# Kernel optimization log

Measured on AMD Instinct MI355X. Metric: run time of the kernel, lower is better.

## Reference

```python
import jax, jax.numpy as jnp
import numpy as np

N = 100000      # nodes
E = 1600000     # edges (unique, no self-loops)
DIN = 128
DOUT = 128


def _make_edges():
    """Unique undirected edges, no self-loops, ring guarantees min degree 2.
    Ensures dense-adjacency semantics == edge-list segment-sum semantics."""
    rng = np.random.default_rng(0)
    ring = np.stack([np.arange(N, dtype=np.int64), (np.arange(N, dtype=np.int64) + 1) % N], axis=1)
    ring = np.sort(ring, axis=1)  # canonical (min,max)
    ring_keys = ring[:, 0] * N + ring[:, 1]
    cand = rng.integers(0, N, size=(3 * E, 2), dtype=np.int64)
    cand = cand[cand[:, 0] != cand[:, 1]]
    cand = np.sort(cand, axis=1)
    keys = cand[:, 0] * N + cand[:, 1]
    _, idx = np.unique(keys, return_index=True)
    cand = cand[np.sort(idx)]
    cand = cand[~np.isin(cand[:, 0] * N + cand[:, 1], ring_keys)][: E - N]
    edges = np.concatenate([ring, cand], axis=0)  # [E, 2]
    return edges.T  # [2, E]


def setup_inputs() -> dict:
    key = jax.random.key(0)
    kx, kw = jax.random.split(key)
    X = jax.random.normal(kx, (N, DIN), dtype=jnp.float32)
    # kaiming_normal_ default (fan_in mode): std = sqrt(2 / fan_in)
    W = jax.random.normal(kw, (DIN, DOUT), dtype=jnp.float32) * np.float32(np.sqrt(2.0 / DIN))
    edge_list = jnp.asarray(_make_edges(), dtype=jnp.int64)
    return {"X": X, "W": W, "edge_list": edge_list}


def reference(X, W, edge_list):
    src, dst = edge_list[0], edge_list[1]
    n = X.shape[0]
    ones = jnp.ones(src.shape[0], dtype=X.dtype)
    # D: each edge increments both endpoint degrees (matches the torch loop)
    deg = jnp.zeros((n,), X.dtype).at[src].add(ones).at[dst].add(ones)
    # A_hat @ X = symmetric neighbor aggregation + self (identity)
    agg = jnp.zeros_like(X).at[dst].add(X[src]).at[src].add(X[dst]) + X
    # D^-1 is inverse of diagonal -> elementwise reciprocal
    z = (agg / deg[:, None]) @ W
    return jax.nn.relu(z)
```

## Files before the change

kernel.cpp:

```cpp
#include <hip/hip_runtime.h>
#include <hip/hip_fp16.h>


#define DFEAT 128
#define BSH 7
#define BNODES (1 << BSH)
#define NBMAX 800
#define EPT_SC 4
#define EPB (1024 * EPT_SC)
#define SORT_CAP 6144

typedef __attribute__((ext_vector_type(8))) short short8;
typedef __attribute__((ext_vector_type(4))) float f32x4;

__device__ __forceinline__ unsigned short f2bf(float x) {
  unsigned u = __float_as_uint(x);
  return (unsigned short)((u + 0x7FFFu + ((u >> 16) & 1u)) >> 16);
}
__device__ __forceinline__ __half2 u2h(unsigned x) {
  union { unsigned u; __half2 h; } c; c.u = x; return c.h;
}
__device__ __forceinline__ unsigned h2u(__half2 x) {
  union { __half2 h; unsigned u; } c; c.h = x; return c.u;
}

__global__ void init_kernel(const int* el32, int* gcur, int* flag, int NB) {
  int i = blockIdx.x * blockDim.x + threadIdx.x;
  if (i < NB) gcur[i] = 0;
  if (i == 0) flag[0] = (el32[1] == 0 && el32[3] == 0) ? 1 : 0;
}

__device__ __forceinline__ int edge_at(const void* el, long long i, int mode64) {
  if (mode64) return (int)((const long long*)el)[i];
  return ((const int*)el)[i];
}

__global__ __launch_bounds__(1024) void scatter_kernel(const void* el,
                                                       const int* __restrict__ flag,
                                                       int* __restrict__ gcur,
                                                       unsigned int* __restrict__ bucket,
                                                       int E, int NB) {
  __shared__ int lh[NBMAX];
  __shared__ int lb[NBMAX];
  int t = threadIdx.x;
  for (int i = t; i < NB; i += 1024) lh[i] = 0;
  __syncthreads();
  int m = flag[0];
  long long e0 = (long long)blockIdx.x * EPB + t;
  int s[EPT_SC], d[EPT_SC];
#pragma unroll
  for (int r = 0; r < EPT_SC; r++) {
    long long e = e0 + r * 1024;
    if (e < E) {
      s[r] = edge_at(el, e, m);
      d[r] = edge_at(el, (long long)E + e, m);
    } else {
      s[r] = -1;
    }
  }
#pragma unroll
  for (int r = 0; r < EPT_SC; r++) {
    if (s[r] >= 0) {
      atomicAdd(&lh[s[r] >> BSH], 1);
      atomicAdd(&lh[d[r] >> BSH], 1);
    }
  }
  __syncthreads();
  for (int i = t; i < NB; i += 1024) {
    int c = lh[i];
    lb[i] = c ? atomicAdd(&gcur[i], c) : 0;
  }
  __syncthreads();
  for (int i = t; i < NB; i += 1024) lh[i] = 0;
  __syncthreads();
#pragma unroll
  for (int r = 0; r < EPT_SC; r++) {
    if (s[r] >= 0) {
      int bs = s[r] >> BSH, bd = d[r] >> BSH;
      int ps = lb[bs] + atomicAdd(&lh[bs], 1);
      if (ps < SORT_CAP)
        bucket[(long long)bs * SORT_CAP + ps] =
            ((unsigned)(s[r] & (BNODES - 1)) << 20) | (unsigned)d[r];
      int pd = lb[bd] + atomicAdd(&lh[bd], 1);
      if (pd < SORT_CAP)
        bucket[(long long)bd * SORT_CAP + pd] =
            ((unsigned)(d[r] & (BNODES - 1)) << 20) | (unsigned)s[r];
    }
  }
}

__global__ __launch_bounds__(1024) void sort_kernel(const unsigned int* __restrict__ bucket,
                                                    const int* __restrict__ gcur,
                                                    int* __restrict__ adj,
                                                    int* __restrict__ start,
                                                    int* __restrict__ degg,
                                                    int n) {
  __shared__ int srt[SORT_CAP];
  __shared__ int h[BNODES], pref[BNODES], cur[BNODES], scn[BNODES];
  int b = blockIdx.x, t = threadIdx.x;
  int cnt = gcur[b]; if (cnt > SORT_CAP) cnt = SORT_CAP;
  long long base = (long long)b * SORT_CAP;

  if (t < BNODES) h[t] = 0;
  __syncthreads();
  for (int i = t; i < cnt; i += 1024)
    atomicAdd(&h[bucket[base + i] >> 20], 1);
  __syncthreads();
  int v = (t < BNODES) ? h[t] : 0;
  if (t < BNODES) scn[t] = v;
  __syncthreads();
  for (int dd = 1; dd < BNODES; dd <<= 1) {
    int a = (t < BNODES && t >= dd) ? scn[t - dd] : 0;
    __syncthreads();
    if (t < BNODES) scn[t] += a;
    __syncthreads();
  }
  if (t < BNODES) { pref[t] = scn[t] - v; cur[t] = scn[t] - v; }
  __syncthreads();
  for (int i = t; i < cnt; i += 1024) {
    unsigned e = bucket[base + i];
    int p = atomicAdd(&cur[e >> 20], 1);
    srt[p] = (int)(e & 0xFFFFFu);
  }
  __syncthreads();
  for (int i = t; i < cnt; i += 1024) adj[base + i] = srt[i];
  int node = (b << BSH) + t;
  if (t < BNODES && node < n) {
    start[node] = (int)(base + pref[t]);
    degg[node] = h[t];
  }
}

__global__ __launch_bounds__(256) void wfrag_kernel(const float* __restrict__ W,
                                                    unsigned int* __restrict__ Wfrag) {
  int e = blockIdx.x * 256 + threadIdx.x;
  if (e >= 2048) return;
  int lane = e & 63;
  int nt = (e >> 6) & 7;
  int kc = e >> 9;
  int k0 = kc * 32 + (lane >> 4) * 8;
  int col = nt * 16 + (lane & 15);
  unsigned int o[4];
#pragma unroll
  for (int jj = 0; jj < 4; jj++) {
    unsigned short lo = f2bf(W[(k0 + 2 * jj) * DFEAT + col]);
    unsigned short hi = f2bf(W[(k0 + 2 * jj + 1) * DFEAT + col]);
    o[jj] = (unsigned)lo | ((unsigned)hi << 16);
  }
  uint4* dst = (uint4*)Wfrag;
  uint4 v; v.x = o[0]; v.y = o[1]; v.z = o[2]; v.w = o[3];
  dst[e] = v;
}

__global__ __launch_bounds__(256) void gemm_kernel(const float* __restrict__ X,
                                                   const short8* __restrict__ Wfrag,
                                                   __half* __restrict__ Yh, int n) {
  int wave = threadIdx.x >> 6;
  int lane = threadIdx.x & 63;
  int row0 = (blockIdx.x * 4 + wave) * 16;
  if (row0 >= n) return;

  int rowA = row0 + (lane & 15);
  if (rowA >= n) rowA = n - 1;
  const float4* Xrow = (const float4*)(X + (long long)rowA * DFEAT);
  int koff = (lane >> 4) * 2;

  f32x4 acc[8];
#pragma unroll
  for (int ntp = 0; ntp < 8; ntp++) acc[ntp] = (f32x4){0.f, 0.f, 0.f, 0.f};

#pragma unroll
  for (int kc = 0; kc < 4; kc++) {
    float4 xa = Xrow[kc * 8 + koff];
    float4 xb = Xrow[kc * 8 + koff + 1];
    short8 a8;
    a8[0] = (short)f2bf(xa.x); a8[1] = (short)f2bf(xa.y);
    a8[2] = (short)f2bf(xa.z); a8[3] = (short)f2bf(xa.w);
    a8[4] = (short)f2bf(xb.x); a8[5] = (short)f2bf(xb.y);
    a8[6] = (short)f2bf(xb.z); a8[7] = (short)f2bf(xb.w);
#pragma unroll
    for (int nt = 0; nt < 8; nt++) {
      short8 b8 = Wfrag[(kc * 8 + nt) * 64 + lane];
      acc[nt] = __builtin_amdgcn_mfma_f32_16x16x32_bf16(a8, b8, acc[nt], 0, 0, 0);
    }
  }

  int rbase = row0 + (lane >> 4) * 4;
  int cbase = lane & 15;
#pragma unroll
  for (int nt = 0; nt < 8; nt++) {
#pragma unroll
    for (int r = 0; r < 4; r++) {
      int row = rbase + r;
      if (row < n)
        Yh[(long long)row * DFEAT + nt * 16 + cbase] = __float2half(acc[nt][r]);
    }
  }
}

__global__ __launch_bounds__(256) void gather_kernel(const uint2* __restrict__ Yh2,
                                                     const int* __restrict__ start,
                                                     const int* __restrict__ degg,
                                                     const int* __restrict__ adj,
                                                     float4* __restrict__ out4, int n) {
  int wid = (int)((blockIdx.x * (long long)blockDim.x + threadIdx.x) >> 6);
  int lane = threadIdx.x & 63;
  if (wid >= n) return;

  int off0 = start[wid], len = degg[wid];
  int c = lane & 31;
  int half = lane >> 5;
  __half2 acc0 = u2h(0), acc1 = u2h(0), acc2 = u2h(0), acc3 = u2h(0);

  for (int base = 0; base < len; base += 64) {
    int cnt = len - base; if (cnt > 64) cnt = 64;
    int idx = (lane < cnt) ? adj[off0 + base + lane] : 0;
    int tt = 0;
    for (; tt + 16 <= cnt; tt += 16) {
      uint2 v[8];
#pragma unroll
      for (int u = 0; u < 8; u++) {
        int j = __shfl(idx, tt + 2 * u + half);
        v[u] = Yh2[(long long)j * 32 + c];
      }
      acc0 = __hadd2(acc0, u2h(v[0].x)); acc1 = __hadd2(acc1, u2h(v[0].y));
      acc2 = __hadd2(acc2, u2h(v[1].x)); acc3 = __hadd2(acc3, u2h(v[1].y));
      acc0 = __hadd2(acc0, u2h(v[2].x)); acc1 = __hadd2(acc1, u2h(v[2].y));
      acc2 = __hadd2(acc2, u2h(v[3].x)); acc3 = __hadd2(acc3, u2h(v[3].y));
      acc0 = __hadd2(acc0, u2h(v[4].x)); acc1 = __hadd2(acc1, u2h(v[4].y));
      acc2 = __hadd2(acc2, u2h(v[5].x)); acc3 = __hadd2(acc3, u2h(v[5].y));
      acc0 = __hadd2(acc0, u2h(v[6].x)); acc1 = __hadd2(acc1, u2h(v[6].y));
      acc2 = __hadd2(acc2, u2h(v[7].x)); acc3 = __hadd2(acc3, u2h(v[7].y));
    }
    for (; tt + 2 <= cnt; tt += 2) {
      int j = __shfl(idx, tt + half);
      uint2 v = Yh2[(long long)j * 32 + c];
      acc0 = __hadd2(acc0, u2h(v.x)); acc1 = __hadd2(acc1, u2h(v.y));
    }
    if (tt < cnt) {
      int j = __shfl(idx, tt);
      uint2 v = Yh2[(long long)j * 32 + c];
      if (half) { v.x = 0; v.y = 0; }
      acc2 = __hadd2(acc2, u2h(v.x)); acc3 = __hadd2(acc3, u2h(v.y));
    }
  }

  acc0 = __hadd2(acc0, acc2);
  acc1 = __hadd2(acc1, acc3);
  acc0 = __hadd2(acc0, u2h((unsigned)__shfl_xor((int)h2u(acc0), 32)));
  acc1 = __hadd2(acc1, u2h((unsigned)__shfl_xor((int)h2u(acc1), 32)));
  uint2 sv = Yh2[(long long)wid * 32 + c];
  acc0 = __hadd2(acc0, u2h(sv.x));
  acc1 = __hadd2(acc1, u2h(sv.y));

  if (half == 0) {
    float2 f0 = __half22float2(acc0);
    float2 f1 = __half22float2(acc1);
    float inv = 1.0f / (float)len;
    float4 o;
    o.x = f0.x * inv; o.y = f0.y * inv; o.z = f1.x * inv; o.w = f1.y * inv;
    o.x = o.x > 0.f ? o.x : 0.f;
    o.y = o.y > 0.f ? o.y : 0.f;
    o.z = o.z > 0.f ? o.z : 0.f;
    o.w = o.w > 0.f ? o.w : 0.f;
    out4[(long long)wid * 32 + c] = o;
  }
}

extern "C" void kernel_launch(void* const* d_in, const int* in_sizes, int n_in,
                              void* d_out, int out_size, void* d_ws, size_t ws_size,
                              hipStream_t stream) {
  const float* X = (const float*)d_in[0];
  const float* W = (const float*)d_in[1];
  const void* el = d_in[2];
  float* out = (float*)d_out;

  int n = in_sizes[0] / DFEAT;
  int E = in_sizes[2] / 2;
  int NB = (n + BNODES - 1) >> BSH;

  char* p = (char*)d_ws;
  auto alloc = [&](size_t bytes) -> char* {
    char* q = p;
    p += (bytes + 511) & ~(size_t)511;
    return q;
  };
  int* gcur = (int*)alloc((size_t)NBMAX * 4);
  int* flag = (int*)alloc(64);
  unsigned int* bucket = (unsigned int*)alloc((size_t)NBMAX * SORT_CAP * 4);
  int* adj   = (int*)alloc((size_t)NBMAX * SORT_CAP * 4);
  int* start = (int*)alloc((size_t)n * 4);
  int* degg  = (int*)alloc((size_t)n * 4);
  unsigned int* Wfrag = (unsigned int*)alloc((size_t)2048 * 16);
  __half* Yh = (__half*)alloc((size_t)n * DFEAT * 2);

  int eblocks = (E + EPB - 1) / EPB;

  init_kernel<<<(NBMAX + 255) / 256, 256, 0, stream>>>((const int*)el, gcur, flag, NB);
  scatter_kernel<<<eblocks, 1024, 0, stream>>>(el, flag, gcur, bucket, E, NB);
  sort_kernel<<<NB, 1024, 0, stream>>>(bucket, gcur, adj, start, degg, n);
  wfrag_kernel<<<8, 256, 0, stream>>>(W, Wfrag);
  gemm_kernel<<<(n + 63) / 64, 256, 0, stream>>>(X, (const short8*)Wfrag, Yh, n);
  gather_kernel<<<(n + 3) / 4, 256, 0, stream>>>((const uint2*)Yh, start, degg, adj,
                                                 (float4*)out, n);
}
```

Measured before the change: 259.2 us.

## Stage bucket scatter in shared memory and write coalesced 32-entry slot chunks

The scatter kernel now buckets each block's edge entries locally in LDS using a block-wide prefix scan, then writes each bucket's run out contiguously to global memory in 32-entry slot chunks padded with sentinel values. This replaces the scattered per-entry global writes that went through global atomic cursors. The W fragment conversion and the 64-bit index detection are folded into the scatter kernel, and the init kernel is replaced by a memset, which cuts kernel launches. In exchange the bucket buffer and LDS use grow, the sort kernel must skip sentinels, and the 1024-wide scan adds barriers.

After: 273.7 us. 5.6% more time.

```diff
diff --git a/kernel.cpp b/kernel.cpp
--- a/kernel.cpp
+++ b/kernel.cpp
@@ -5,10 +5,13 @@
 #define DFEAT 128
 #define BSH 7
 #define BNODES (1 << BSH)
-#define NBMAX 800
-#define EPT_SC 4
-#define EPB (1024 * EPT_SC)
+#define NBMAX 784
+#define EPB 8192
+#define ENTB (2 * EPB)
+#define SLOT_CAPS 256
+#define BCAP (SLOT_CAPS * 32)
 #define SORT_CAP 6144
+#define SENT 0xFFFFFFFFu
 
 typedef __attribute__((ext_vector_type(8))) short short8;
 typedef __attribute__((ext_vector_type(4))) float f32x4;
@@ -24,32 +27,54 @@
   union { __half2 h; unsigned u; } c; c.h = x; return c.u;
 }
 
-__global__ void init_kernel(const int* el32, int* gcur, int* flag, int NB) {
-  int i = blockIdx.x * blockDim.x + threadIdx.x;
-  if (i < NB) gcur[i] = 0;
-  if (i == 0) flag[0] = (el32[1] == 0 && el32[3] == 0) ? 1 : 0;
-}
-
 __device__ __forceinline__ int edge_at(const void* el, long long i, int mode64) {
   if (mode64) return (int)((const long long*)el)[i];
   return ((const int*)el)[i];
 }
 
 __global__ __launch_bounds__(1024) void scatter_kernel(const void* el,
-                                                       const int* __restrict__ flag,
-                                                       int* __restrict__ gcur,
+                                                       int* __restrict__ scur,
                                                        unsigned int* __restrict__ bucket,
+                                                       const float* __restrict__ W,
+                                                       unsigned int* __restrict__ Wfrag,
                                                        int E, int NB) {
-  __shared__ int lh[NBMAX];
-  __shared__ int lb[NBMAX];
+  __shared__ unsigned staged[ENTB];
+  __shared__ int lh[NBMAX], lbase[NBMAX], gbe[NBMAX];
+  __shared__ int scanbuf[1024];
   int t = threadIdx.x;
+
+  if (blockIdx.x == 0) {
+#pragma unroll
+    for (int rr = 0; rr < 2; rr++) {
+      int e = t + rr * 1024;
+      int lane = e & 63;
+      int nt = (e >> 6) & 7;
+      int kc = e >> 9;
+      int k0 = kc * 32 + (lane >> 4) * 8;
+      int col = nt * 16 + (lane & 15);
+      unsigned int o[4];
+#pragma unroll
+      for (int jj = 0; jj < 4; jj++) {
+        unsigned short lo = f2bf(W[(k0 + 2 * jj) * DFEAT + col]);
+        unsigned short hi = f2bf(W[(k0 + 2 * jj + 1) * DFEAT + col]);
+        o[jj] = (unsigned)lo | ((unsigned)hi << 16);
+      }
+      uint4* dst = (uint4*)Wfrag;
+      uint4 v; v.x = o[0]; v.y = o[1]; v.z = o[2]; v.w = o[3];
+      dst[e] = v;
+    }
+  }
+
+  const int* el32 = (const int*)el;
+  int m = (el32[1] == 0 && el32[3] == 0) ? 1 : 0;
+
   for (int i = t; i < NB; i += 1024) lh[i] = 0;
   __syncthreads();
-  int m = flag[0];
+
   long long e0 = (long long)blockIdx.x * EPB + t;
-  int s[EPT_SC], d[EPT_SC];
-#pragma unroll
-  for (int r = 0; r < EPT_SC; r++) {
+  int s[8], d[8];
+#pragma unroll
+  for (int r = 0; r < 8; r++) {
     long long e = e0 + r * 1024;
     if (e < E) {
       s[r] = edge_at(el, e, m);
@@ -59,38 +84,60 @@
     }
   }
 #pragma unroll
-  for (int r = 0; r < EPT_SC; r++) {
+  for (int r = 0; r < 8; r++) {
     if (s[r] >= 0) {
       atomicAdd(&lh[s[r] >> BSH], 1);
       atomicAdd(&lh[d[r] >> BSH], 1);
     }
   }
   __syncthreads();
-  for (int i = t; i < NB; i += 1024) {
-    int c = lh[i];
-    lb[i] = c ? atomicAdd(&gcur[i], c) : 0;
-  }
-  __syncthreads();
-  for (int i = t; i < NB; i += 1024) lh[i] = 0;
-  __syncthreads();
-#pragma unroll
-  for (int r = 0; r < EPT_SC; r++) {
+
+  int v = (t < NB) ? lh[t] : 0;
+  scanbuf[t] = v;
+  __syncthreads();
+  for (int dd = 1; dd < 1024; dd <<= 1) {
+    int a = (t >= dd) ? scanbuf[t - dd] : 0;
+    __syncthreads();
+    scanbuf[t] += a;
+    __syncthreads();
+  }
+  if (t < NB) lbase[t] = scanbuf[t] - v;
+  if (t < NB) {
+    int slots = (v + 31) >> 5;
+    gbe[t] = slots ? (atomicAdd(&scur[t], slots) << 5) : 0;
+  }
+  __syncthreads();
+  scanbuf[t] = 0;
+  __syncthreads();
+
+#pragma unroll
+  for (int r = 0; r < 8; r++) {
     if (s[r] >= 0) {
       int bs = s[r] >> BSH, bd = d[r] >> BSH;
-      int ps = lb[bs] + atomicAdd(&lh[bs], 1);
-      if (ps < SORT_CAP)
-        bucket[(long long)bs * SORT_CAP + ps] =
-            ((unsigned)(s[r] & (BNODES - 1)) << 20) | (unsigned)d[r];
-      int pd = lb[bd] + atomicAdd(&lh[bd], 1);
-      if (pd < SORT_CAP)
-        bucket[(long long)bd * SORT_CAP + pd] =
-            ((unsigned)(d[r] & (BNODES - 1)) << 20) | (unsigned)s[r];
+      int ps = lbase[bs] + atomicAdd(&scanbuf[bs], 1);
+      staged[ps] = ((unsigned)(s[r] & (BNODES - 1)) << 20) | (unsigned)d[r];
+      int pd = lbase[bd] + atomicAdd(&scanbuf[bd], 1);
+      staged[pd] = ((unsigned)(d[r] & (BNODES - 1)) << 20) | (unsigned)s[r];
+    }
+  }
+  __syncthreads();
+
+  int wave = t >> 6, lane = t & 63;
+  for (int i = wave; i < NB; i += 16) {
+    int cnt = lh[i];
+    if (cnt == 0) continue;
+    int lb = lbase[i], gb = gbe[i];
+    int padded = ((cnt + 31) >> 5) << 5;
+    long long bb = (long long)i * BCAP;
+    for (int j = lane; j < padded; j += 64) {
+      if (gb + j < BCAP)
+        bucket[bb + gb + j] = (j < cnt) ? staged[lb + j] : SENT;
     }
   }
 }
 
 __global__ __launch_bounds__(1024) void sort_kernel(const unsigned int* __restrict__ bucket,
-                                                    const int* __restrict__ gcur,
+                                                    const int* __restrict__ scur,
                                                     int* __restrict__ adj,
                                                     int* __restrict__ start,
                                                     int* __restrict__ degg,
@@ -98,13 +145,16 @@
   __shared__ int srt[SORT_CAP];
   __shared__ int h[BNODES], pref[BNODES], cur[BNODES], scn[BNODES];
   int b = blockIdx.x, t = threadIdx.x;
-  int cnt = gcur[b]; if (cnt > SORT_CAP) cnt = SORT_CAP;
-  long long base = (long long)b * SORT_CAP;
+  int slots = scur[b]; if (slots > SLOT_CAPS) slots = SLOT_CAPS;
+  int cnt = slots << 5;
+  long long base = (long long)b * BCAP;
 
   if (t < BNODES) h[t] = 0;
   __syncthreads();
-  for (int i = t; i < cnt; i += 1024)
-    atomicAdd(&h[bucket[base + i] >> 20], 1);
+  for (int i = t; i < cnt; i += 1024) {
+    unsigned e = bucket[base + i];
+    if (e != SENT) atomicAdd(&h[e >> 20], 1);
+  }
   __syncthreads();
   int v = (t < BNODES) ? h[t] : 0;
   if (t < BNODES) scn[t] = v;
@@ -119,37 +169,20 @@
   __syncthreads();
   for (int i = t; i < cnt; i += 1024) {
     unsigned e = bucket[base + i];
-    int p = atomicAdd(&cur[e >> 20], 1);
-    srt[p] = (int)(e & 0xFFFFFu);
-  }
-  __syncthreads();
-  for (int i = t; i < cnt; i += 1024) adj[base + i] = srt[i];
+    if (e != SENT) {
+      int p = atomicAdd(&cur[e >> 20], 1);
+      if (p < SORT_CAP) srt[p] = (int)(e & 0xFFFFFu);
+    }
+  }
+  __syncthreads();
+  int total = scn[BNODES - 1]; if (total > SORT_CAP) total = SORT_CAP;
+  long long abase = (long long)b * SORT_CAP;
+  for (int i = t; i < total; i += 1024) adj[abase + i] = srt[i];
   int node = (b << BSH) + t;
   if (t < BNODES && node < n) {
-    start[node] = (int)(base + pref[t]);
+    start[node] = (int)(abase + pref[t]);
     degg[node] = h[t];
   }
-}
-
-__global__ __launch_bounds__(256) void wfrag_kernel(const float* __restrict__ W,
-                                                    unsigned int* __restrict__ Wfrag) {
-  int e = blockIdx.x * 256 + threadIdx.x;
-  if (e >= 2048) return;
-  int lane = e & 63;
-  int nt = (e >> 6) & 7;
-  int kc = e >> 9;
-  int k0 = kc * 32 + (lane >> 4) * 8;
-  int col = nt * 16 + (lane & 15);
-  unsigned int o[4];
-#pragma unroll
-  for (int jj = 0; jj < 4; jj++) {
-    unsigned short lo = f2bf(W[(k0 + 2 * jj) * DFEAT + col]);
-    unsigned short hi = f2bf(W[(k0 + 2 * jj + 1) * DFEAT + col]);
-    o[jj] = (unsigned)lo | ((unsigned)hi << 16);
-  }
-  uint4* dst = (uint4*)Wfrag;
-  uint4 v; v.x = o[0]; v.y = o[1]; v.z = o[2]; v.w = o[3];
-  dst[e] = v;
 }
 
 __global__ __launch_bounds__(256) void gemm_kernel(const float* __restrict__ X,
@@ -285,9 +318,8 @@
     p += (bytes + 511) & ~(size_t)511;
     return q;
   };
-  int* gcur = (int*)alloc((size_t)NBMAX * 4);
-  int* flag = (int*)alloc(64);
-  unsigned int* bucket = (unsigned int*)alloc((size_t)NBMAX * SORT_CAP * 4);
+  int* scur = (int*)alloc((size_t)NBMAX * 4);
+  unsigned int* bucket = (unsigned int*)alloc((size_t)NBMAX * BCAP * 4);
   int* adj   = (int*)alloc((size_t)NBMAX * SORT_CAP * 4);
   int* start = (int*)alloc((size_t)n * 4);
   int* degg  = (int*)alloc((size_t)n * 4);
@@ -296,10 +328,9 @@
 
   int eblocks = (E + EPB - 1) / EPB;
 
-  init_kernel<<<(NBMAX + 255) / 256, 256, 0, stream>>>((const int*)el, gcur, flag, NB);
-  scatter_kernel<<<eblocks, 1024, 0, stream>>>(el, flag, gcur, bucket, E, NB);
-  sort_kernel<<<NB, 1024, 0, stream>>>(bucket, gcur, adj, start, degg, n);
-  wfrag_kernel<<<8, 256, 0, stream>>>(W, Wfrag);
+  hipMemsetAsync(scur, 0, (size_t)NBMAX * 4, stream);
+  scatter_kernel<<<eblocks, 1024, 0, stream>>>(el, scur, bucket, W, Wfrag, E, NB);
+  sort_kernel<<<NB, 1024, 0, stream>>>(bucket, scur, adj, start, degg, n);
   gemm_kernel<<<(n + 63) / 64, 256, 0, stream>>>(X, (const short8*)Wfrag, Yh, n);
   gather_kernel<<<(n + 3) / 4, 256, 0, stream>>>((const uint2*)Yh, start, degg, adj,
                                                  (float4*)out, n);
```

## Merge edge scatter and feature GEMM into one heterogeneous launch

Applied to the files above, without the earlier changes.

Combines the edge-bucketing scatter and the X·W bf16 MFMA GEMM into a single kernel whose blocks take either role depending on block index, so the two independent stages can run at the same time and fewer kernels are launched. The W fragment conversion moves into each GEMM block's shared memory instead of a separate kernel and global buffer, and the init kernel is replaced by a memset plus an inline 64-bit-index check. Block size drops to 512 with 8 edges per thread, and each GEMM block now covers 128 rows. In exchange, every GEMM block recomputes the W fragments and the mixed block roles may balance unevenly across CUs.

Result: faster. 252.5 us (-2.6%).

```diff
diff --git a/kernel.cpp b/kernel.cpp
--- a/kernel.cpp
+++ b/kernel.cpp
@@ -5,10 +5,11 @@
 #define DFEAT 128
 #define BSH 7
 #define BNODES (1 << BSH)
-#define NBMAX 800
-#define EPT_SC 4
-#define EPB (1024 * EPT_SC)
+#define NBMAX 784
+#define EPT_SC 8
+#define EPB (512 * EPT_SC)
 #define SORT_CAP 6144
+#define GROWS 128
 
 typedef __attribute__((ext_vector_type(8))) short short8;
 typedef __attribute__((ext_vector_type(4))) float f32x4;
@@ -23,68 +24,126 @@
 __device__ __forceinline__ unsigned h2u(__half2 x) {
   union { __half2 h; unsigned u; } c; c.h = x; return c.u;
 }
-
-__global__ void init_kernel(const int* el32, int* gcur, int* flag, int NB) {
-  int i = blockIdx.x * blockDim.x + threadIdx.x;
-  if (i < NB) gcur[i] = 0;
-  if (i == 0) flag[0] = (el32[1] == 0 && el32[3] == 0) ? 1 : 0;
-}
-
 __device__ __forceinline__ int edge_at(const void* el, long long i, int mode64) {
   if (mode64) return (int)((const long long*)el)[i];
   return ((const int*)el)[i];
 }
 
-__global__ __launch_bounds__(1024) void scatter_kernel(const void* el,
-                                                       const int* __restrict__ flag,
-                                                       int* __restrict__ gcur,
-                                                       unsigned int* __restrict__ bucket,
-                                                       int E, int NB) {
-  __shared__ int lh[NBMAX];
-  __shared__ int lb[NBMAX];
+union SMemW {
+  struct { int lh[NBMAX]; int lb[NBMAX]; } sc;
+  uint4 wf[2048];
+};
+
+__global__ __launch_bounds__(512, 4) void work_kernel(
+    const void* el, int* __restrict__ gcur, unsigned int* __restrict__ bucket,
+    const float* __restrict__ X, const float* __restrict__ W,
+    __half* __restrict__ Yh, int E, int n, int NB, int SBLKS) {
+  __shared__ SMemW sm;
   int t = threadIdx.x;
-  for (int i = t; i < NB; i += 1024) lh[i] = 0;
-  __syncthreads();
-  int m = flag[0];
-  long long e0 = (long long)blockIdx.x * EPB + t;
-  int s[EPT_SC], d[EPT_SC];
-#pragma unroll
-  for (int r = 0; r < EPT_SC; r++) {
-    long long e = e0 + r * 1024;
-    if (e < E) {
-      s[r] = edge_at(el, e, m);
-      d[r] = edge_at(el, (long long)E + e, m);
-    } else {
-      s[r] = -1;
-    }
-  }
-#pragma unroll
-  for (int r = 0; r < EPT_SC; r++) {
-    if (s[r] >= 0) {
-      atomicAdd(&lh[s[r] >> BSH], 1);
-      atomicAdd(&lh[d[r] >> BSH], 1);
-    }
-  }
-  __syncthreads();
-  for (int i = t; i < NB; i += 1024) {
-    int c = lh[i];
-    lb[i] = c ? atomicAdd(&gcur[i], c) : 0;
-  }
-  __syncthreads();
-  for (int i = t; i < NB; i += 1024) lh[i] = 0;
-  __syncthreads();
-#pragma unroll
-  for (int r = 0; r < EPT_SC; r++) {
-    if (s[r] >= 0) {
-      int bs = s[r] >> BSH, bd = d[r] >> BSH;
-      int ps = lb[bs] + atomicAdd(&lh[bs], 1);
-      if (ps < SORT_CAP)
-        bucket[(long long)bs * SORT_CAP + ps] =
-            ((unsigned)(s[r] & (BNODES - 1)) << 20) | (unsigned)d[r];
-      int pd = lb[bd] + atomicAdd(&lh[bd], 1);
-      if (pd < SORT_CAP)
-        bucket[(long long)bd * SORT_CAP + pd] =
-            ((unsigned)(d[r] & (BNODES - 1)) << 20) | (unsigned)s[r];
+
+  if ((int)blockIdx.x < SBLKS) {
+    const int* el32 = (const int*)el;
+    int m = (el32[1] == 0 && el32[3] == 0) ? 1 : 0;
+    for (int i = t; i < NB; i += 512) sm.sc.lh[i] = 0;
+    __syncthreads();
+    long long e0 = (long long)blockIdx.x * EPB + t;
+    int s[EPT_SC], d[EPT_SC];
+#pragma unroll
+    for (int r = 0; r < EPT_SC; r++) {
+      long long e = e0 + r * 512;
+      if (e < E) {
+        s[r] = edge_at(el, e, m);
+        d[r] = edge_at(el, (long long)E + e, m);
+      } else {
+        s[r] = -1;
+      }
+    }
+#pragma unroll
+    for (int r = 0; r < EPT_SC; r++) {
+      if (s[r] >= 0) {
+        atomicAdd(&sm.sc.lh[s[r] >> BSH], 1);
+        atomicAdd(&sm.sc.lh[d[r] >> BSH], 1);
+      }
+    }
+    __syncthreads();
+    for (int i = t; i < NB; i += 512) {
+      int c = sm.sc.lh[i];
+      sm.sc.lb[i] = c ? atomicAdd(&gcur[i], c) : 0;
+    }
+    __syncthreads();
+    for (int i = t; i < NB; i += 512) sm.sc.lh[i] = 0;
+    __syncthreads();
+#pragma unroll
+    for (int r = 0; r < EPT_SC; r++) {
+      if (s[r] >= 0) {
+        int bs = s[r] >> BSH, bd = d[r] >> BSH;
+        int ps = sm.sc.lb[bs] + atomicAdd(&sm.sc.lh[bs], 1);
+        if (ps < SORT_CAP)
+          bucket[(long long)bs * SORT_CAP + ps] =
+              ((unsigned)(s[r] & (BNODES - 1)) << 20) | (unsigned)d[r];
+        int pd = sm.sc.lb[bd] + atomicAdd(&sm.sc.lh[bd], 1);
+        if (pd < SORT_CAP)
+          bucket[(long long)bd * SORT_CAP + pd] =
+              ((unsigned)(d[r] & (BNODES - 1)) << 20) | (unsigned)s[r];
+      }
+    }
+  } else {
+    int gb = blockIdx.x - SBLKS;
+    for (int e = t; e < 2048; e += 512) {
+      int l = e & 63;
+      int nt = (e >> 6) & 7;
+      int kc = e >> 9;
+      int k0 = kc * 32 + (l >> 4) * 8;
+      int col = nt * 16 + (l & 15);
+      unsigned int o[4];
+#pragma unroll
+      for (int jj = 0; jj < 4; jj++) {
+        unsigned short lo = f2bf(W[(k0 + 2 * jj) * DFEAT + col]);
+        unsigned short hi = f2bf(W[(k0 + 2 * jj + 1) * DFEAT + col]);
+        o[jj] = (unsigned)lo | ((unsigned)hi << 16);
+      }
+      uint4 v; v.x = o[0]; v.y = o[1]; v.z = o[2]; v.w = o[3];
+      sm.wf[e] = v;
+    }
+    __syncthreads();
+    const short8* Wf8 = (const short8*)sm.wf;
+    int wave = t >> 6, lane = t & 63;
+    int row0 = gb * GROWS + wave * 16;
+    if (row0 < n) {
+      int rowA = row0 + (lane & 15);
+      if (rowA >= n) rowA = n - 1;
+      const float4* Xrow = (const float4*)(X + (long long)rowA * DFEAT);
+      int koff = (lane >> 4) * 2;
+
+      f32x4 acc[8];
+#pragma unroll
+      for (int ntp = 0; ntp < 8; ntp++) acc[ntp] = (f32x4){0.f, 0.f, 0.f, 0.f};
+#pragma unroll
+      for (int kc = 0; kc < 4; kc++) {
+        float4 xa = Xrow[kc * 8 + koff];
+        float4 xb = Xrow[kc * 8 + koff + 1];
+        short8 a8;
+        a8[0] = (short)f2bf(xa.x); a8[1] = (short)f2bf(xa.y);
+        a8[2] = (short)f2bf(xa.z); a8[3] = (short)f2bf(xa.w);
+        a8[4] = (short)f2bf(xb.x); a8[5] = (short)f2bf(xb.y);
+        a8[6] = (short)f2bf(xb.z); a8[7] = (short)f2bf(xb.w);
+#pragma unroll
+        for (int nt = 0; nt < 8; nt++) {
+          short8 b8 = Wf8[(kc * 8 + nt) * 64 + lane];
+          acc[nt] = __builtin_amdgcn_mfma_f32_16x16x32_bf16(a8, b8, acc[nt], 0, 0, 0);
+        }
+      }
+      int rbase = row0 + (lane >> 4) * 4;
+      int cbase = lane & 15;
+#pragma unroll
+      for (int nt = 0; nt < 8; nt++) {
+#pragma unroll
+        for (int r = 0; r < 4; r++) {
+          int row = rbase + r;
+          if (row < n)
+            Yh[(long long)row * DFEAT + nt * 16 + cbase] = __float2half(acc[nt][r]);
+        }
+      }
     }
   }
 }
@@ -131,73 +190,6 @@
   }
 }
 
-__global__ __launch_bounds__(256) void wfrag_kernel(const float* __restrict__ W,
-                                                    unsigned int* __restrict__ Wfrag) {
-  int e = blockIdx.x * 256 + threadIdx.x;
-  if (e >= 2048) return;
-  int lane = e & 63;
-  int nt = (e >> 6) & 7;
-  int kc = e >> 9;
-  int k0 = kc * 32 + (lane >> 4) * 8;
-  int col = nt * 16 + (lane & 15);
-  unsigned int o[4];
-#pragma unroll
-  for (int jj = 0; jj < 4; jj++) {
-    unsigned short lo = f2bf(W[(k0 + 2 * jj) * DFEAT + col]);
-    unsigned short hi = f2bf(W[(k0 + 2 * jj + 1) * DFEAT + col]);
-    o[jj] = (unsigned)lo | ((unsigned)hi << 16);
-  }
-  uint4* dst = (uint4*)Wfrag;
-  uint4 v; v.x = o[0]; v.y = o[1]; v.z = o[2]; v.w = o[3];
-  dst[e] = v;
-}
-
-__global__ __launch_bounds__(256) void gemm_kernel(const float* __restrict__ X,
-                                                   const short8* __restrict__ Wfrag,
-                                                   __half* __restrict__ Yh, int n) {
-  int wave = threadIdx.x >> 6;
-  int lane = threadIdx.x & 63;
-  int row0 = (blockIdx.x * 4 + wave) * 16;
-  if (row0 >= n) return;
-
-  int rowA = row0 + (lane & 15);
-  if (rowA >= n) rowA = n - 1;
-  const float4* Xrow = (const float4*)(X + (long long)rowA * DFEAT);
-  int koff = (lane >> 4) * 2;
-
-  f32x4 acc[8];
-#pragma unroll
-  for (int ntp = 0; ntp < 8; ntp++) acc[ntp] = (f32x4){0.f, 0.f, 0.f, 0.f};
-
-#pragma unroll
-  for (int kc = 0; kc < 4; kc++) {
-    float4 xa = Xrow[kc * 8 + koff];
-    float4 xb = Xrow[kc * 8 + koff + 1];
-    short8 a8;
-    a8[0] = (short)f2bf(xa.x); a8[1] = (short)f2bf(xa.y);
-    a8[2] = (short)f2bf(xa.z); a8[3] = (short)f2bf(xa.w);
-    a8[4] = (short)f2bf(xb.x); a8[5] = (short)f2bf(xb.y);
-    a8[6] = (short)f2bf(xb.z); a8[7] = (short)f2bf(xb.w);
-#pragma unroll
-    for (int nt = 0; nt < 8; nt++) {
-      short8 b8 = Wfrag[(kc * 8 + nt) * 64 + lane];
-      acc[nt] = __builtin_amdgcn_mfma_f32_16x16x32_bf16(a8, b8, acc[nt], 0, 0, 0);
-    }
-  }
-
-  int rbase = row0 + (lane >> 4) * 4;
-  int cbase = lane & 15;
-#pragma unroll
-  for (int nt = 0; nt < 8; nt++) {
-#pragma unroll
-    for (int r = 0; r < 4; r++) {
-      int row = rbase + r;
-      if (row < n)
-        Yh[(long long)row * DFEAT + nt * 16 + cbase] = __float2half(acc[nt][r]);
-    }
-  }
-}
-
 __global__ __launch_bounds__(256) void gather_kernel(const uint2* __restrict__ Yh2,
                                                      const int* __restrict__ start,
                                                      const int* __restrict__ degg,
@@ -286,21 +278,19 @@
     return q;
   };
   int* gcur = (int*)alloc((size_t)NBMAX * 4);
-  int* flag = (int*)alloc(64);
   unsigned int* bucket = (unsigned int*)alloc((size_t)NBMAX * SORT_CAP * 4);
   int* adj   = (int*)alloc((size_t)NBMAX * SORT_CAP * 4);
   int* start = (int*)alloc((size_t)n * 4);
   int* degg  = (int*)alloc((size_t)n * 4);
-  unsigned int* Wfrag = (unsigned int*)alloc((size_t)2048 * 16);
   __half* Yh = (__half*)alloc((size_t)n * DFEAT * 2);
 
-  int eblocks = (E + EPB - 1) / EPB;
-
-  init_kernel<<<(NBMAX + 255) / 256, 256, 0, stream>>>((const int*)el, gcur, flag, NB);
-  scatter_kernel<<<eblocks, 1024, 0, stream>>>(el, flag, gcur, bucket, E, NB);
+  int SBLKS = (E + EPB - 1) / EPB;
+  int GBLKS = (n + GROWS - 1) / GROWS;
+
+  hipMemsetAsync(gcur, 0, (size_t)NBMAX * 4, stream);
+  work_kernel<<<SBLKS + GBLKS, 512, 0, stream>>>(el, gcur, bucket, X, W, Yh,
+                                                 E, n, NB, SBLKS);
   sort_kernel<<<NB, 1024, 0, stream>>>(bucket, gcur, adj, start, degg, n);
-  wfrag_kernel<<<8, 256, 0, stream>>>(W, Wfrag);
-  gemm_kernel<<<(n + 63) / 64, 256, 0, stream>>>(X, (const short8*)Wfrag, Yh, n);
   gather_kernel<<<(n + 3) / 4, 256, 0, stream>>>((const uint2*)Yh, start, degg, adj,
                                                  (float4*)out, n);
 }
```
